# Kernel optimization log

Measured on AMD Instinct MI355X. Metric: run time of the kernel, lower is better.

Reference implementation:

```python
import jax, jax.numpy as jnp
from jax import lax
import numpy as np

# pywt Wavelet('db4') decomposition filters
DEC_LO = jnp.array([-0.010597401784997278, 0.032883011666982945, 0.030841381835986965,
                    -0.18703481171888114, -0.027983769416983848, 0.6308807679295904,
                    0.7148465705525415, 0.23037781330885523], dtype=jnp.float32)
DEC_HI = jnp.array([-0.23037781330885523, 0.7148465705525415, -0.6308807679295904,
                    -0.027983769416983848, 0.18703481171888114, 0.030841381835986965,
                    -0.032883011666982945, -0.010597401784997278], dtype=jnp.float32)
FLT = 8
BN_INV = np.float32(1.0 / np.sqrt(1.0 + 1e-5))  # BatchNorm eval: running_mean=0, running_var=1


def dwt_db4(v):
    """Vectorized pywt.dwt(v, 'db4', mode='symmetric') along the last axis.
    v: (..., n) -> (cA, cD), each (..., (n+FLT-1)//2).
    pywt: symmetric-pad by FLT-1, true convolution with filter, take valid[1::2].
    Equivalent: correlate padded[1:...] with flipped filter, stride 2."""
    n = v.shape[-1]
    out_len = (n + FLT - 1) // 2
    xp = jnp.pad(v, [(0, 0)] * (v.ndim - 1) + [(FLT - 1, FLT - 1)], mode='symmetric')
    xp = xp[..., 1:1 + 2 * (out_len - 1) + FLT]
    lead = v.shape[:-1]
    xr = xp.reshape(-1, 1, xp.shape[-1])                      # (N*, 1, L)
    kern = jnp.stack([DEC_LO[::-1], DEC_HI[::-1]])[:, None, :]  # (2, 1, 8)
    y = lax.conv_general_dilated(xr, kern, (2,), 'VALID',
                                 dimension_numbers=('NCH', 'OIH', 'NCH'))
    return y[:, 0].reshape(lead + (out_len,)), y[:, 1].reshape(lead + (out_len,))


def conv_bn_relu(x, w, g, b):
    # x: (B, C, S); w: (O, I, K) no bias; BN in eval mode; ReLU; dropout off (eval)
    k = w.shape[-1]
    p = (k - 1) // 2
    y = lax.conv_general_dilated(x, w, (1,), [(p, p)],
                                 dimension_numbers=('NCH', 'OIH', 'NCH'))
    return jax.nn.relu((g * BN_INV)[None, :, None] * y + b[None, :, None])


def setup_inputs() -> dict:
    key = jax.random.key(0)
    ks = jax.random.split(key, 16)
    C, S, B = 88, 2048, 4
    d = dict()
    d['x'] = jax.random.normal(ks[0], (B, S, C), dtype=jnp.float32)
    d['w1'] = jax.random.normal(ks[1], (C, C, 1), dtype=jnp.float32) * 0.05
    d['w2a'] = jax.random.normal(ks[2], (C, C, 1), dtype=jnp.float32) * 0.05
    d['w2b'] = jax.random.normal(ks[3], (C, C, 3), dtype=jnp.float32) * 0.05
    d['w3a'] = jax.random.normal(ks[4], (C, C, 1), dtype=jnp.float32) * 0.05
    d['w3b'] = jax.random.normal(ks[5], (C, C, 3), dtype=jnp.float32) * 0.05
    d['w3c'] = jax.random.normal(ks[6], (C, C, 5), dtype=jnp.float32) * 0.05
    for nm in ['g1', 'g2a', 'g2b', 'g3a', 'g3b', 'g3c']:
        d[nm] = jnp.ones((C,), dtype=jnp.float32)
    for nm in ['b1', 'b2a', 'b2b', 'b3a', 'b3b', 'b3c']:
        d[nm] = jnp.zeros((C,), dtype=jnp.float32)
    d['Wmp'] = jax.random.normal(ks[7], (C, 3 * C), dtype=jnp.float32) * 0.05
    d['bmp'] = jnp.zeros((C,), dtype=jnp.float32)
    d['Wq'] = jax.random.normal(ks[8], (C, C), dtype=jnp.float32) * 0.1
    d['Wk'] = jax.random.normal(ks[9], (C, C), dtype=jnp.float32) * 0.1
    d['Wv'] = jax.random.normal(ks[10], (C, C), dtype=jnp.float32) * 0.1
    d['Wout'] = jax.random.normal(ks[11], (C, 112), dtype=jnp.float32) * 0.05
    d['bout'] = jnp.zeros((C,), dtype=jnp.float32)
    return d


def reference(x, w1, g1, b1, w2a, g2a, b2a, w2b, g2b, b2b,
              w3a, g3a, b3a, w3b, g3b, b3b, w3c, g3c, b3c,
              Wmp, bmp, Wq, Wk, Wv, Wout, bout):
    B, S, H = x.shape
    head = 4
    dk = H // head                                # 22
    wd = dk // 2 + 3 if dk % 2 == 0 else (dk + 1) // 2 + 3  # 14
    xt = jnp.swapaxes(x, 1, 2)                    # (B, C, S)
    # mutil_Parallel: three conv lines + fuse + residual
    x1 = conv_bn_relu(xt, w1, g1, b1)
    x2 = conv_bn_relu(conv_bn_relu(xt, w2a, g2a, b2a), w2b, g2b, b2b)
    x3 = conv_bn_relu(conv_bn_relu(conv_bn_relu(xt, w3a, g3a, b3a), w3b, g3b, b3b), w3c, g3c, b3c)
    cat = jnp.concatenate([x1, x2, x3], axis=1)   # (B, 3C, S)
    mp = jnp.einsum('bcs,oc->bso', cat, Wmp) + bmp + x  # (B, S, C)
    identity = mp
    # multi-head attention with wavelet-transformed values
    scale = dk ** (-0.5)
    q = jnp.einsum('bsh,oh->bso', mp, Wq).reshape(B, S, head, dk).transpose(0, 2, 1, 3) * scale
    k = jnp.einsum('bsh,oh->bso', mp, Wk).reshape(B, S, head, dk).transpose(0, 2, 1, 3)
    v = jnp.einsum('bsh,oh->bso', mp, Wv).reshape(B, S, head, dk).transpose(0, 2, 1, 3)
    attn = jax.nn.softmax(jnp.einsum('bhqd,bhkd->bhqk', q, k), axis=-1)  # (B,4,S,S)
    cA, cD = dwt_db4(v)                           # each (B, 4, S, 14)
    wcd = jnp.einsum('bhqk,bhkd->bhqd', attn, cD)  # (B, 4, S, 14)
    xo = jax.nn.relu(wcd.transpose(0, 2, 1, 3).reshape(B, S, head * wd))
    cAr = cA.reshape(B, S, head * wd)             # faithful to source's direct .view
    out = jnp.concatenate([xo, cAr], axis=-1) @ Wout.T + bout
    return identity + out
```

## Files before the change

### kernel.cpp

```cpp
#include <hip/hip_runtime.h>

#define BN_INV  0.99999500003749981f
#define QSCALE  0.21320071635561041f

typedef unsigned int uint;
typedef unsigned short u16;
typedef __attribute__((ext_vector_type(8))) short s16x8;
typedef __attribute__((ext_vector_type(4))) float f32x4;

#define OFF_BCAT 0
#define OFF_V    512
#define OFF_MP   721408
#define SW0    2884608
#define SB1    (SW0)
#define SB2B   (SW0+30720)
#define SB3B   (SW0+67584)
#define SB3C   (SW0+104448)
#define SBMP   (SW0+165888)
#define SBQKV  (SW0+202752)
#define SBOUT  (SW0+239616)
#define SXB    3148800
#define SXCAT  3869696
#define SX2    6032384
#define ST3B   6753280
#define SX3    7474176
#define SMPB   8195072
#define SQB    3869696
#define SKB    4918272
#define SCDT   5966848
#define SXOB   6753280

__constant__ float c_dlo[8] = {-0.010597401784997278f, 0.032883011666982945f,
    0.030841381835986965f, -0.18703481171888114f, -0.02798376941698385f,
    0.6308807679295904f, 0.7148465705525415f, 0.23037781330885523f};
__constant__ float c_dhi[8] = {-0.23037781330885523f, 0.7148465705525415f,
    -0.6308807679295904f, -0.02798376941698385f, 0.18703481171888114f,
    0.030841381835986965f, -0.032883011666982945f, -0.010597401784997278f};

__device__ __forceinline__ u16 f2bf(float f) {
    uint u = __float_as_uint(f);
    uint r = u + 0x7fffu + ((u >> 16) & 1u);
    return (u16)(r >> 16);
}

__global__ __launch_bounds__(256) void prepk(
    const float* __restrict__ x,
    const float* __restrict__ w1, const float* __restrict__ w2a, const float* __restrict__ w2b,
    const float* __restrict__ w3a, const float* __restrict__ w3b, const float* __restrict__ w3c,
    const float* __restrict__ g1, const float* __restrict__ g2a, const float* __restrict__ g2b,
    const float* __restrict__ g3a, const float* __restrict__ g3b, const float* __restrict__ g3c,
    const float* __restrict__ b1, const float* __restrict__ b2a, const float* __restrict__ b3a,
    const float* __restrict__ Wmp, const float* __restrict__ Wq, const float* __restrict__ Wk,
    const float* __restrict__ Wv, const float* __restrict__ Wout, float* __restrict__ ws)
{
    u16* wu = (u16*)ws;
    int r = blockIdx.x * 256 + threadIdx.x;
    if (r < 264) {
        ws[OFF_BCAT + r] = (r < 88) ? b1[r] : (r < 176 ? b2a[r-88] : b3a[r-176]);
        return;
    }
    r -= 264;
    if (r < 320*96) {
        int n = r / 96, kk = r % 96; float v = 0.f;
        if (kk < 88 && n < 264) {
            if (n < 88)       v = w1 [n*88+kk]       * g1 [n];
            else if (n < 176) v = w2a[(n-88)*88+kk]  * g2a[n-88];
            else              v = w3a[(n-176)*88+kk] * g3a[n-176];
            v *= BN_INV;
        }
        wu[SB1 + r] = f2bf(v); return;
    }
    r -= 320*96;
    if (r < 128*288) {
        int n = r / 288, kk = r % 288, t = kk/96, i = kk%96; float v = 0.f;
        if (n < 88 && i < 88) v = w2b[n*264 + i*3 + t] * g2b[n] * BN_INV;
        wu[SB2B + r] = f2bf(v); return;
    }
    r -= 128*288;
    if (r < 128*288) {
        int n = r / 288, kk = r % 288, t = kk/96, i = kk%96; float v = 0.f;
        if (n < 88 && i < 88) v = w3b[n*264 + i*3 + t] * g3b[n] * BN_INV;
        wu[SB3B + r] = f2bf(v); return;
    }
    r -= 128*288;
    if (r < 128*480) {
        int n = r / 480, kk = r % 480, t = kk/96, i = kk%96; float v = 0.f;
        if (n < 88 && i < 88) v = w3c[n*440 + i*5 + t] * g3c[n] * BN_INV;
        wu[SB3C + r] = f2bf(v); return;
    }
    r -= 128*480;
    if (r < 128*288) {
        int n = r / 288, kk = r % 288, c = kk/96, i = kk%96; float v = 0.f;
        if (n < 88 && i < 88) v = Wmp[n*264 + c*88 + i];
        wu[SBMP + r] = f2bf(v); return;
    }
    r -= 128*288;
    if (r < 384*96) {
        int n = r / 96, kk = r % 96, sec = n / 128, o = n % 128; float v = 0.f;
        if (o < 88 && kk < 88) {
            if (sec == 0)      v = Wq[o*88+kk] * QSCALE;
            else if (sec == 1) v = Wk[o*88+kk];
            else               v = Wv[o*88+kk];
        }
        wu[SBQKV + r] = f2bf(v); return;
    }
    r -= 384*96;
    if (r < 128*192) {
        int n = r / 192, kk = r % 192; float v = 0.f;
        if (n < 88 && kk < 112) v = Wout[n*112 + kk];
        wu[SBOUT + r] = f2bf(v); return;
    }
    r -= 128*192;
    if (r < 8192*88) {
        wu[SXB + r] = f2bf(x[r]); return;
    }
}

struct GemmChunks {
    int soff[5];
    int stride[5];
    int shift[5];
    int cols[5];
};

template<int NCH, int MODE, int OUTM>
__global__ __launch_bounds__(256) void gemmk(GemmChunks ch,
    const u16* __restrict__ wsrc,
    const u16* __restrict__ Bw, const u16* __restrict__ Bw2, int Ktot,
    const float* __restrict__ bias, const float* __restrict__ bias2,
    const float* __restrict__ resid, int relu,
    u16* __restrict__ outb, u16* __restrict__ outb2,
    float* __restrict__ outf, int outStride, int N)
{
    __shared__ u16 As[64*104];
    __shared__ u16 Bs[64*104];
    int tid = threadIdx.x;
    int lane = tid & 63, w = tid >> 6, wr = w >> 1, wc = w & 1;
    int p0 = blockIdx.x * 64;
    int nb = blockIdx.y;
    int which = (MODE == 2) ? (nb >> 1) : 0;
    int nbl   = (MODE == 2) ? (nb & 1) : nb;
    const u16* Bw_ = (MODE == 2 && which) ? Bw2 : Bw;
    int bs = p0 & ~2047, be = bs + 2048;

    f32x4 acc[2][2];
    #pragma unroll
    for (int a = 0; a < 2; a++)
        #pragma unroll
        for (int b = 0; b < 2; b++) acc[a][b] = (f32x4){0.f,0.f,0.f,0.f};

    int ar0 = (wr*32 + (lane&15))*104 + (lane>>4)*8;
    int br0 = (wc*32 + (lane&15))*104 + (lane>>4)*8;

    int4 ra[3], rb[3];
    auto loadC = [&](int c) {
        int soff = ch.soff[c] + which*88;
        int stride = ch.stride[c], shift = ch.shift[c], cols = ch.cols[c];
        #pragma unroll
        for (int t = 0; t < 3; t++) {
            int e = tid + t*256;
            int r = e / 12, seg = e % 12;
            int row = p0 + r + shift;
            int4 v = {0,0,0,0};
            if (row >= bs && row < be && seg*8 < cols)
                v = *(const int4*)&wsrc[(size_t)soff + (size_t)row*stride + seg*8];
            ra[t] = v;
            rb[t] = *(const int4*)&Bw_[((size_t)(nbl*64 + r))*Ktot + c*96 + seg*8];
        }
    };

    loadC(0);
    for (int c = 0; c < NCH; c++) {
        #pragma unroll
        for (int t = 0; t < 3; t++) {
            int e = tid + t*256;
            int r = e / 12, seg = e % 12;
            *(int4*)&As[r*104 + seg*8] = ra[t];
            *(int4*)&Bs[r*104 + seg*8] = rb[t];
        }
        __syncthreads();
        if (c + 1 < NCH) loadC(c + 1);
        #pragma unroll
        for (int ks = 0; ks < 3; ks++) {
            s16x8 a0 = *(const s16x8*)&As[ar0 + ks*32];
            s16x8 a1 = *(const s16x8*)&As[ar0 + 16*104 + ks*32];
            s16x8 b0 = *(const s16x8*)&Bs[br0 + ks*32];
            s16x8 b1 = *(const s16x8*)&Bs[br0 + 16*104 + ks*32];
            acc[0][0] = __builtin_amdgcn_mfma_f32_16x16x32_bf16(a0, b0, acc[0][0], 0, 0, 0);
            acc[0][1] = __builtin_amdgcn_mfma_f32_16x16x32_bf16(a0, b1, acc[0][1], 0, 0, 0);
            acc[1][0] = __builtin_amdgcn_mfma_f32_16x16x32_bf16(a1, b0, acc[1][0], 0, 0, 0);
            acc[1][1] = __builtin_amdgcn_mfma_f32_16x16x32_bf16(a1, b1, acc[1][1], 0, 0, 0);
        }
        __syncthreads();
    }

    int rbase = p0 + wr*32 + (lane>>4)*4;
    if (MODE != 1) {
        u16* outb_ = (MODE == 2 && which) ? outb2 : outb;
        const float* bias_ = (MODE == 2 && which) ? bias2 : bias;
        int cbase = nbl*64 + wc*32 + (lane&15);
        #pragma unroll
        for (int fn = 0; fn < 2; fn++) {
            int col = cbase + fn*16;
            if (col < N) {
                float bb = bias_ ? bias_[col] : 0.f;
                #pragma unroll
                for (int fm = 0; fm < 2; fm++)
                    #pragma unroll
                    for (int j = 0; j < 4; j++) {
                        int row = rbase + fm*16 + j;
                        float v = acc[fm][fn][j] + bb;
                        if (relu) v = fmaxf(v, 0.f);
                        if (resid) v += resid[(size_t)row*outStride + col];
                        if (OUTM & 1) outb_[(size_t)row*outStride + col] = f2bf(v);
                        if (OUTM & 2) outf[(size_t)row*outStride + col] = v;
                    }
            }
        }
    } else {
        u16* wq = outb;
        int sec = nb >> 1;
        #pragma unroll
        for (int fn = 0; fn < 2; fn++) {
            int cw = (nb&1)*64 + wc*32 + fn*16 + (lane&15);
            if (cw < 88) {
                int h = cw / 22, d = cw % 22;
                #pragma unroll
                for (int fm = 0; fm < 2; fm++)
                    #pragma unroll
                    for (int j = 0; j < 4; j++) {
                        int row = rbase + fm*16 + j;
                        int b = row >> 11, s = row & 2047;
                        float v = acc[fm][fn][j];
                        if (sec == 0)
                            wq[SQB + ((size_t)(b*4+h)*2048 + s)*32 + d] = f2bf(v);
                        else if (sec == 1)
                            wq[SKB + ((size_t)(b*4+h)*2048 + s)*32 + d] = f2bf(v);
                        else
                            outf[OFF_V + (size_t)row*88 + cw] = v;
                    }
            }
        }
    }
}

__global__ __launch_bounds__(256) void dwtk(float* __restrict__ ws)
{
    u16* wu = (u16*)ws;
    int tid = threadIdx.x;
    int p0 = blockIdx.x * 16;
    const float* V = ws + OFF_V;
    for (int e = tid; e < 896; e += 256) {
        int p = e / 56, rr = e % 56, h = rr / 14, jj = rr % 14;
        int pos = p0 + p, b = pos >> 11, s = pos & 2047;
        const float* v = &V[(size_t)pos*88 + h*22];
        float ca = 0.f, cd = 0.f;
        #pragma unroll
        for (int t = 0; t < 8; t++) {
            int pp = 1 + 2*jj + t;
            int oi = pp < 7 ? 6 - pp : (pp < 29 ? pp - 7 : 50 - pp);
            float vv = v[oi];
            ca = fmaf(vv, c_dlo[7-t], ca);
            cd = fmaf(vv, c_dhi[7-t], cd);
        }
        wu[SCDT + ((size_t)((b*4+h)*16 + jj))*2048 + s] = f2bf(cd);
        int hs = h*2048 + s, s2 = hs >> 2, qd = hs & 3;
        wu[SXOB + ((size_t)b*2048 + s2)*112 + 56 + qd*14 + jj] = f2bf(ca);
    }
    uint* wi = (uint*)ws;
    for (int e = tid; e < 640; e += 256) {
        int p = e / 40, t = e % 40;
        int h = t / 10, rest = t % 10, arr = rest / 5, ui = rest % 5;
        int pos = p0 + p, b = pos >> 11, s = pos & 2047;
        size_t base = (size_t)((arr ? SKB : SQB) >> 1) + ((size_t)(b*4+h)*2048 + s)*16;
        wi[base + 11 + ui] = 0;
    }
    for (int e = tid; e < 128; e += 256) {
        int p = e / 8, t = e % 8, h = t >> 1, dd = 14 + (t & 1);
        int pos = p0 + p, b = pos >> 11, s = pos & 2047;
        wu[SCDT + ((size_t)((b*4+h)*16 + dd))*2048 + s] = 0;
    }
}

__global__ __launch_bounds__(512, 4) void attnk(float* __restrict__ ws)
{
    const u16* wu = (const u16*)ws;
    u16* wua = (u16*)ws;
    __shared__ __align__(16) u16 Kt[2*64*40];
    __shared__ __align__(16) u16 CDt[2*16*72];
    __shared__ __align__(16) u16 Pb[8][16*72];
    __shared__ float cb[8][16];
    int tid = threadIdx.x, lane = tid & 63, w = tid >> 6;
    int bh = blockIdx.y;
    int qsub = w & 3, half = w >> 2;
    int q0 = blockIdx.x * 64 + qsub * 16;
    int qrow = lane & 15, grp = lane >> 4;

    s16x8 qf = *(const s16x8*)&wu[SQB + ((size_t)bh*2048 + q0 + qrow)*32 + grp*8];
    const u16* Kbase = wu + SKB + (size_t)bh*2048*32;
    const u16* Cbase = wu + SCDT + (size_t)bh*16*2048;
    const u16* Kh = &Kt[half*2560];
    const u16* Ch = &CDt[half*1152];

    f32x4 o = (f32x4){0.f,0.f,0.f,0.f};
    float m = -1e30f, l = 0.f;

    for (int kt = 0; kt < 16; kt++) {
        __syncthreads();
        {
            int hh = tid >> 8, rr = (tid >> 2) & 63, seg = tid & 3;
            *(int4*)&Kt[hh*2560 + rr*40 + seg*8] =
                *(const int4*)&Kbase[(size_t)(hh*1024 + kt*64 + rr)*32 + seg*8];
        }
        if (tid < 256) {
            int hh = tid >> 7, d = (tid >> 3) & 15, seg = tid & 7;
            *(int4*)&CDt[hh*1152 + d*72 + seg*8] =
                *(const int4*)&Cbase[(size_t)d*2048 + hh*1024 + kt*64 + seg*8];
        }
        __syncthreads();

        f32x4 s4[4];
        #pragma unroll
        for (int sub = 0; sub < 4; sub++) {
            s16x8 kf = *(const s16x8*)&Kh[(sub*16 + qrow)*40 + grp*8];
            s4[sub] = __builtin_amdgcn_mfma_f32_16x16x32_bf16(kf, qf,
                        (f32x4){0.f,0.f,0.f,0.f}, 0, 0, 0);
        }
        float sv[16];
        #pragma unroll
        for (int sub = 0; sub < 4; sub++)
            #pragma unroll
            for (int j = 0; j < 4; j++) sv[sub*4+j] = s4[sub][j];

        float mx[8];
        #pragma unroll
        for (int i = 0; i < 8; i++) mx[i] = fmaxf(sv[i], sv[i+8]);
        #pragma unroll
        for (int i = 0; i < 4; i++) mx[i] = fmaxf(mx[i], mx[i+4]);
        float tm = fmaxf(fmaxf(mx[0], mx[1]), fmaxf(mx[2], mx[3]));
        tm = fmaxf(tm, __shfl_xor(tm, 16));
        tm = fmaxf(tm, __shfl_xor(tm, 32));

        if (!__all(tm <= m + 8.f)) {
            float mn = fmaxf(m, tm);
            float corr = __expf(m - mn);
            m = mn; l *= corr;
            if (lane < 16) cb[w][lane] = corr;
            __builtin_amdgcn_s_waitcnt(0);
            const float* cp = &cb[w][grp*4];
            #pragma unroll
            for (int j = 0; j < 4; j++) o[j] *= cp[j];
        }

        float pv[16];
        #pragma unroll
        for (int i = 0; i < 16; i++) pv[i] = __expf(sv[i] - m);
        float sm[8];
        #pragma unroll
        for (int i = 0; i < 8; i++) sm[i] = pv[i] + pv[i+8];
        #pragma unroll
        for (int i = 0; i < 4; i++) sm[i] += sm[i+4];
        float ls = (sm[0] + sm[1]) + (sm[2] + sm[3]);
        ls += __shfl_xor(ls, 16);
        ls += __shfl_xor(ls, 32);
        l += ls;

        {
            uint* pb32 = (uint*)Pb[w];
            #pragma unroll
            for (int sub = 0; sub < 4; sub++) {
                uint u01 = (uint)f2bf(pv[sub*4+0]) | ((uint)f2bf(pv[sub*4+1]) << 16);
                uint u23 = (uint)f2bf(pv[sub*4+2]) | ((uint)f2bf(pv[sub*4+3]) << 16);
                int sa = qrow*72 + sub*16 + grp*4;
                *(uint2*)&pb32[sa >> 1] = make_uint2(u01, u23);
            }
        }
        #pragma unroll
        for (int ks = 0; ks < 2; ks++) {
            s16x8 pa = *(const s16x8*)&Pb[w][qrow*72 + ks*32 + grp*8];
            s16x8 cf = *(const s16x8*)&Ch[qrow*72 + ks*32 + grp*8];
            o = __builtin_amdgcn_mfma_f32_16x16x32_bf16(pa, cf, o, 0, 0, 0);
        }
    }

    __syncthreads();
    float* part = (float*)Kt;
    if (lane < 16) { part[(w*16+lane)*18 + 0] = m; part[(w*16+lane)*18 + 1] = l; }
    #pragma unroll
    for (int j = 0; j < 4; j++) part[(w*16 + grp*4 + j)*18 + 2 + qrow] = o[j];
    __syncthreads();
    if (w < 4) {
        int q = qrow;
        const float* pa = &part[(w*16 + q)*18];
        const float* pb = &part[((w+4)*16 + q)*18];
        float m0 = pa[0], l0 = pa[1], m1 = pb[0], l1 = pb[1];
        float M = fmaxf(m0, m1);
        float e0 = __expf(m0 - M), e1 = __expf(m1 - M);
        float inv = 1.f / (l0*e0 + l1*e1);
        int b = bh >> 2, h = bh & 3;
        int s = blockIdx.x * 64 + w * 16 + q;
        #pragma unroll
        for (int dd = 0; dd < 4; dd++) {
            int d = grp*4 + dd;
            if (d < 14) {
                float val = (pa[2+d]*e0 + pb[2+d]*e1) * inv;
                wua[SXOB + ((size_t)b*2048 + s)*112 + h*14 + d] = f2bf(fmaxf(val, 0.f));
            }
        }
    }
}

extern "C" void kernel_launch(void* const* d_in, const int* in_sizes, int n_in,
                              void* d_out, int out_size, void* d_ws, size_t ws_size,
                              hipStream_t stream) {
    const float* x    = (const float*)d_in[0];
    const float* w1   = (const float*)d_in[1];
    const float* w2a  = (const float*)d_in[2];
    const float* w2b  = (const float*)d_in[3];
    const float* w3a  = (const float*)d_in[4];
    const float* w3b  = (const float*)d_in[5];
    const float* w3c  = (const float*)d_in[6];
    const float* g1   = (const float*)d_in[7];
    const float* g2a  = (const float*)d_in[8];
    const float* g2b  = (const float*)d_in[9];
    const float* g3a  = (const float*)d_in[10];
    const float* g3b  = (const float*)d_in[11];
    const float* g3c  = (const float*)d_in[12];
    const float* b1   = (const float*)d_in[13];
    const float* b2a  = (const float*)d_in[14];
    const float* b2b  = (const float*)d_in[15];
    const float* b3a  = (const float*)d_in[16];
    const float* b3b  = (const float*)d_in[17];
    const float* b3c  = (const float*)d_in[18];
    const float* Wmp  = (const float*)d_in[19];
    const float* bmp  = (const float*)d_in[20];
    const float* Wq   = (const float*)d_in[21];
    const float* Wk   = (const float*)d_in[22];
    const float* Wv   = (const float*)d_in[23];
    const float* Wout = (const float*)d_in[24];
    const float* bout = (const float*)d_in[25];
    float* ws = (float*)d_ws;
    float* out = (float*)d_out;
    u16* wu = (u16*)d_ws;

    prepk<<<3850, 256, 0, stream>>>(x, w1, w2a, w2b, w3a, w3b, w3c,
                                    g1, g2a, g2b, g3a, g3b, g3c,
                                    b1, b2a, b3a, Wmp, Wq, Wk, Wv, Wout, ws);

    {
        GemmChunks c{}; c.soff[0]=SXB; c.stride[0]=88; c.shift[0]=0; c.cols[0]=88;
        gemmk<1,0,1><<<dim3(128,5), 256, 0, stream>>>(c, wu, wu+SB1, nullptr, 96,
            ws+OFF_BCAT, nullptr, nullptr, 1, wu+SXCAT, nullptr, nullptr, 264, 264);
    }
    {
        GemmChunks c{};
        for (int t = 0; t < 3; t++) { c.soff[t]=SXCAT+88; c.stride[t]=264; c.shift[t]=t-1; c.cols[t]=88; }
        gemmk<3,2,1><<<dim3(128,4), 256, 0, stream>>>(c, wu, wu+SB2B, wu+SB3B, 288,
            b2b, b3b, nullptr, 1, wu+SX2, wu+ST3B, nullptr, 88, 88);
    }
    {
        GemmChunks c{};
        for (int t = 0; t < 5; t++) { c.soff[t]=ST3B; c.stride[t]=88; c.shift[t]=t-2; c.cols[t]=88; }
        gemmk<5,0,1><<<dim3(128,2), 256, 0, stream>>>(c, wu, wu+SB3C, nullptr, 480,
            b3c, nullptr, nullptr, 1, wu+SX3, nullptr, nullptr, 88, 88);
    }
    {
        GemmChunks c{};
        c.soff[0]=SXCAT; c.stride[0]=264; c.shift[0]=0; c.cols[0]=88;
        c.soff[1]=SX2;   c.stride[1]=88;  c.shift[1]=0; c.cols[1]=88;
        c.soff[2]=SX3;   c.stride[2]=88;  c.shift[2]=0; c.cols[2]=88;
        gemmk<3,0,3><<<dim3(128,2), 256, 0, stream>>>(c, wu, wu+SBMP, nullptr, 288,
            bmp, nullptr, x, 0, wu+SMPB, nullptr, ws+OFF_MP, 88, 88);
    }
    {
        GemmChunks c{}; c.soff[0]=SMPB; c.stride[0]=88; c.shift[0]=0; c.cols[0]=88;
        gemmk<1,1,0><<<dim3(128,6), 256, 0, stream>>>(c, wu, wu+SBQKV, nullptr, 96,
            nullptr, nullptr, nullptr, 0, wu, nullptr, ws, 0, 0);
    }
    dwtk<<<512, 256, 0, stream>>>(ws);
    attnk<<<dim3(32, 16), 512, 0, stream>>>(ws);
    {
        GemmChunks c{};
        c.soff[0]=SXOB;    c.stride[0]=112; c.shift[0]=0; c.cols[0]=96;
        c.soff[1]=SXOB+96; c.stride[1]=112; c.shift[1]=0; c.cols[1]=16;
        gemmk<2,0,2><<<dim3(128,2), 256, 0, stream>>>(c, wu, wu+SBOUT, nullptr, 192,
            bout, nullptr, ws+OFF_MP, 0, nullptr, nullptr, out, 88, 88);
    }
}
```

Baseline: 202.9 us.

## Split attention keys four ways, stage DWT input in LDS, move pad zeroing to GEMM

The attention kernel now gives each block 32 queries and splits the key range into four quarters across wave pairs. This doubles the grid to 1024 blocks and halves the serial key-tile loop, and the four partial softmax states are merged at the end. The DWT kernel stages 32 positions of V in shared memory with coalesced loads before computing the coefficients. Zeroing of the Q/K padding columns moves into the QKV GEMM epilogue, which removes scattered writes from the DWT kernel. In exchange, each block reloads its Q tile, uses more shared memory, and does a heavier four-way combine.

```diff
diff --git a/kernel.cpp b/kernel.cpp
--- a/kernel.cpp
+++ b/kernel.cpp
@@ -239,6 +239,17 @@
                         else
                             outf[OFF_V + (size_t)row*88 + cw] = v;
                     }
+            } else if (sec < 2 && cw < 128) {
+                int t = cw - 88, h = t / 10, dpad = 22 + t % 10;
+                size_t sqk = (sec == 0) ? (size_t)SQB : (size_t)SKB;
+                #pragma unroll
+                for (int fm = 0; fm < 2; fm++)
+                    #pragma unroll
+                    for (int j = 0; j < 4; j++) {
+                        int row = rbase + fm*16 + j;
+                        int b = row >> 11, s = row & 2047;
+                        wq[sqk + ((size_t)(b*4+h)*2048 + s)*32 + dpad] = 0;
+                    }
             }
         }
     }
@@ -247,13 +258,22 @@
 __global__ __launch_bounds__(256) void dwtk(float* __restrict__ ws)
 {
     u16* wu = (u16*)ws;
+    __shared__ float vs[32*89];
     int tid = threadIdx.x;
-    int p0 = blockIdx.x * 16;
+    int p0 = blockIdx.x * 32;
     const float* V = ws + OFF_V;
-    for (int e = tid; e < 896; e += 256) {
-        int p = e / 56, rr = e % 56, h = rr / 14, jj = rr % 14;
-        int pos = p0 + p, b = pos >> 11, s = pos & 2047;
-        const float* v = &V[(size_t)pos*88 + h*22];
+    for (int e = tid; e < 32*88; e += 256) {
+        int p = e / 88, c = e - p*88;
+        vs[p*89 + c] = V[(size_t)p0*88 + e];
+    }
+    __syncthreads();
+    int b = p0 >> 11, sbase = p0 & 2047;
+    #pragma unroll
+    for (int it = 0; it < 7; it++) {
+        int idx = it*256 + tid;
+        int p = idx & 31, hjj = idx >> 5;
+        int h = hjj / 14, jj = hjj - h*14;
+        const float* v = &vs[p*89 + h*22];
         float ca = 0.f, cd = 0.f;
         #pragma unroll
         for (int t = 0; t < 8; t++) {
@@ -263,22 +283,15 @@
             ca = fmaf(vv, c_dlo[7-t], ca);
             cd = fmaf(vv, c_dhi[7-t], cd);
         }
+        int s = sbase + p;
         wu[SCDT + ((size_t)((b*4+h)*16 + jj))*2048 + s] = f2bf(cd);
         int hs = h*2048 + s, s2 = hs >> 2, qd = hs & 3;
         wu[SXOB + ((size_t)b*2048 + s2)*112 + 56 + qd*14 + jj] = f2bf(ca);
     }
-    uint* wi = (uint*)ws;
-    for (int e = tid; e < 640; e += 256) {
-        int p = e / 40, t = e % 40;
-        int h = t / 10, rest = t % 10, arr = rest / 5, ui = rest % 5;
-        int pos = p0 + p, b = pos >> 11, s = pos & 2047;
-        size_t base = (size_t)((arr ? SKB : SQB) >> 1) + ((size_t)(b*4+h)*2048 + s)*16;
-        wi[base + 11 + ui] = 0;
-    }
-    for (int e = tid; e < 128; e += 256) {
-        int p = e / 8, t = e % 8, h = t >> 1, dd = 14 + (t & 1);
-        int pos = p0 + p, b = pos >> 11, s = pos & 2047;
-        wu[SCDT + ((size_t)((b*4+h)*16 + dd))*2048 + s] = 0;
+    {
+        int p = tid & 31, t = tid >> 5;
+        int h = t >> 1, dd = 14 + (t & 1);
+        wu[SCDT + ((size_t)((b*4+h)*16 + dd))*2048 + sbase + p] = 0;
     }
 }
 
@@ -286,36 +299,38 @@
 {
     const u16* wu = (const u16*)ws;
     u16* wua = (u16*)ws;
-    __shared__ __align__(16) u16 Kt[2*64*40];
-    __shared__ __align__(16) u16 CDt[2*16*72];
+    __shared__ __align__(16) u16 Kt[4*64*40];
+    __shared__ __align__(16) u16 CDt[4*16*72];
     __shared__ __align__(16) u16 Pb[8][16*72];
     __shared__ float cb[8][16];
     int tid = threadIdx.x, lane = tid & 63, w = tid >> 6;
     int bh = blockIdx.y;
-    int qsub = w & 3, half = w >> 2;
-    int q0 = blockIdx.x * 64 + qsub * 16;
+    int qsub = w & 1, quar = w >> 1;
+    int q0 = blockIdx.x * 32 + qsub * 16;
     int qrow = lane & 15, grp = lane >> 4;
 
     s16x8 qf = *(const s16x8*)&wu[SQB + ((size_t)bh*2048 + q0 + qrow)*32 + grp*8];
     const u16* Kbase = wu + SKB + (size_t)bh*2048*32;
     const u16* Cbase = wu + SCDT + (size_t)bh*16*2048;
-    const u16* Kh = &Kt[half*2560];
-    const u16* Ch = &CDt[half*1152];
+    const u16* Kh = &Kt[quar*2560];
+    const u16* Ch = &CDt[quar*1152];
 
     f32x4 o = (f32x4){0.f,0.f,0.f,0.f};
     float m = -1e30f, l = 0.f;
 
-    for (int kt = 0; kt < 16; kt++) {
+    for (int kt = 0; kt < 8; kt++) {
         __syncthreads();
+        #pragma unroll
+        for (int t = 0; t < 2; t++) {
+            int e = tid + t*512;
+            int qq = e >> 8, rr = (e >> 2) & 63, seg = e & 3;
+            *(int4*)&Kt[qq*2560 + rr*40 + seg*8] =
+                *(const int4*)&Kbase[(size_t)(qq*512 + kt*64 + rr)*32 + seg*8];
+        }
         {
-            int hh = tid >> 8, rr = (tid >> 2) & 63, seg = tid & 3;
-            *(int4*)&Kt[hh*2560 + rr*40 + seg*8] =
-                *(const int4*)&Kbase[(size_t)(hh*1024 + kt*64 + rr)*32 + seg*8];
-        }
-        if (tid < 256) {
-            int hh = tid >> 7, d = (tid >> 3) & 15, seg = tid & 7;
-            *(int4*)&CDt[hh*1152 + d*72 + seg*8] =
-                *(const int4*)&Cbase[(size_t)d*2048 + hh*1024 + kt*64 + seg*8];
+            int qq = tid >> 7, d = (tid >> 3) & 15, seg = tid & 7;
+            *(int4*)&CDt[qq*1152 + d*72 + seg*8] =
+                *(const int4*)&Cbase[(size_t)d*2048 + qq*512 + kt*64 + seg*8];
         }
         __syncthreads();
 
@@ -389,23 +404,28 @@
     #pragma unroll
     for (int j = 0; j < 4; j++) part[(w*16 + grp*4 + j)*18 + 2 + qrow] = o[j];
     __syncthreads();
-    if (w < 4) {
+    if (w < 2) {
         int q = qrow;
-        const float* pa = &part[(w*16 + q)*18];
-        const float* pb = &part[((w+4)*16 + q)*18];
-        float m0 = pa[0], l0 = pa[1], m1 = pb[0], l1 = pb[1];
-        float M = fmaxf(m0, m1);
-        float e0 = __expf(m0 - M), e1 = __expf(m1 - M);
-        float inv = 1.f / (l0*e0 + l1*e1);
+        float M = -1e30f;
+        #pragma unroll
+        for (int qt = 0; qt < 4; qt++) M = fmaxf(M, part[((qt*2+w)*16 + q)*18]);
+        float L = 0.f, v[4] = {0.f,0.f,0.f,0.f};
+        #pragma unroll
+        for (int qt = 0; qt < 4; qt++) {
+            const float* pp = &part[((qt*2+w)*16 + q)*18];
+            float ee = __expf(pp[0] - M);
+            L += ee * pp[1];
+            #pragma unroll
+            for (int dd = 0; dd < 4; dd++) v[dd] += ee * pp[2 + grp*4 + dd];
+        }
+        float inv = 1.f / L;
         int b = bh >> 2, h = bh & 3;
-        int s = blockIdx.x * 64 + w * 16 + q;
+        int s = blockIdx.x * 32 + w * 16 + q;
         #pragma unroll
         for (int dd = 0; dd < 4; dd++) {
             int d = grp*4 + dd;
-            if (d < 14) {
-                float val = (pa[2+d]*e0 + pb[2+d]*e1) * inv;
-                wua[SXOB + ((size_t)b*2048 + s)*112 + h*14 + d] = f2bf(fmaxf(val, 0.f));
-            }
+            if (d < 14)
+                wua[SXOB + ((size_t)b*2048 + s)*112 + h*14 + d] = f2bf(fmaxf(v[dd]*inv, 0.f));
         }
     }
 }
@@ -477,8 +497,8 @@
         gemmk<1,1,0><<<dim3(128,6), 256, 0, stream>>>(c, wu, wu+SBQKV, nullptr, 96,
             nullptr, nullptr, nullptr, 0, wu, nullptr, ws, 0, 0);
     }
-    dwtk<<<512, 256, 0, stream>>>(ws);
-    attnk<<<dim3(32, 16), 512, 0, stream>>>(ws);
+    dwtk<<<256, 256, 0, stream>>>(ws);
+    attnk<<<dim3(64, 16), 512, 0, stream>>>(ws);
     {
         GemmChunks c{};
         c.soff[0]=SXOB;    c.stride[0]=112; c.shift[0]=0; c.cols[0]=96;
```

Measured after the change: 204.9 us. About the same (+1.0%).

## Stage GEMM conv halos in LDS once, prefetch attention tiles, stage DWT input

Applied to the files above, without the earlier changes.

The conv-as-GEMM kernel now loads the whole input tile plus a halo of neighbouring rows, and all weight chunks, into shared memory in one pass. Each shifted tap then reuses those rows instead of reloading shifted copies per chunk, and the per-chunk barriers go away. The attention kernel register-prefetches the next K and CD tiles and broadcasts the softmax correction with a shuffle instead of through shared memory. The DWT kernel stages V rows in shared memory, processes 32 positions per block, and moves zeroing of the Q/K padding columns into the QKV GEMM epilogue. The costs are more shared memory per GEMM block, which may lower occupancy, and the loss of load/compute overlap inside the GEMM.

```diff
diff --git a/kernel.cpp b/kernel.cpp
--- a/kernel.cpp
+++ b/kernel.cpp
@@ -119,21 +119,23 @@
 struct GemmChunks {
     int soff[5];
     int stride[5];
-    int shift[5];
     int cols[5];
 };
 
-template<int NCH, int MODE, int OUTM>
+template<int NCH, int HALO, int MODE, int OUTM>
 __global__ __launch_bounds__(256) void gemmk(GemmChunks ch,
     const u16* __restrict__ wsrc,
-    const u16* __restrict__ Bw, const u16* __restrict__ Bw2, int Ktot,
+    const u16* __restrict__ Bw, const u16* __restrict__ Bw2,
     const float* __restrict__ bias, const float* __restrict__ bias2,
     const float* __restrict__ resid, int relu,
     u16* __restrict__ outb, u16* __restrict__ outb2,
     float* __restrict__ outf, int outStride, int N)
 {
-    __shared__ u16 As[64*104];
-    __shared__ u16 Bs[64*104];
+    constexpr int RA   = HALO ? (64 + NCH - 1) : 64 * NCH;
+    constexpr int BSTR = NCH * 96 + 8;
+    constexpr int KTOT = NCH * 96;
+    __shared__ u16 As[RA * 104];
+    __shared__ u16 Bs[64 * BSTR];
     int tid = threadIdx.x;
     int lane = tid & 63, w = tid >> 6, wr = w >> 1, wc = w & 1;
     int p0 = blockIdx.x * 64;
@@ -143,6 +145,36 @@
     const u16* Bw_ = (MODE == 2 && which) ? Bw2 : Bw;
     int bs = p0 & ~2047, be = bs + 2048;
 
+    if (HALO) {
+        constexpr int OFS = (NCH - 1) / 2;
+        int soff = ch.soff[0] + which * 88;
+        int stride = ch.stride[0], cols = ch.cols[0];
+        for (int e = tid; e < RA * 12; e += 256) {
+            int r = e / 12, seg = e % 12;
+            int row = p0 + r - OFS;
+            int4 v = {0,0,0,0};
+            if (row >= bs && row < be && seg*8 < cols)
+                v = *(const int4*)&wsrc[(size_t)soff + (size_t)row*stride + seg*8];
+            *(int4*)&As[r*104 + seg*8] = v;
+        }
+    } else {
+        for (int e = tid; e < NCH * 768; e += 256) {
+            int c = e / 768, rem = e - c*768;
+            int r = rem / 12, seg = rem % 12;
+            int row = p0 + r;
+            int4 v = {0,0,0,0};
+            if (seg*8 < ch.cols[c])
+                v = *(const int4*)&wsrc[(size_t)ch.soff[c] + (size_t)row*ch.stride[c] + seg*8];
+            *(int4*)&As[c*6656 + r*104 + seg*8] = v;
+        }
+    }
+    for (int e = tid; e < 64 * NCH * 12; e += 256) {
+        int n = e / (NCH*12), seg = e % (NCH*12);
+        *(int4*)&Bs[n*BSTR + seg*8] =
+            *(const int4*)&Bw_[((size_t)(nbl*64 + n))*KTOT + seg*8];
+    }
+    __syncthreads();
+
     f32x4 acc[2][2];
     #pragma unroll
     for (int a = 0; a < 2; a++)
@@ -150,48 +182,23 @@
         for (int b = 0; b < 2; b++) acc[a][b] = (f32x4){0.f,0.f,0.f,0.f};
 
     int ar0 = (wr*32 + (lane&15))*104 + (lane>>4)*8;
-    int br0 = (wc*32 + (lane&15))*104 + (lane>>4)*8;
-
-    int4 ra[3], rb[3];
-    auto loadC = [&](int c) {
-        int soff = ch.soff[c] + which*88;
-        int stride = ch.stride[c], shift = ch.shift[c], cols = ch.cols[c];
-        #pragma unroll
-        for (int t = 0; t < 3; t++) {
-            int e = tid + t*256;
-            int r = e / 12, seg = e % 12;
-            int row = p0 + r + shift;
-            int4 v = {0,0,0,0};
-            if (row >= bs && row < be && seg*8 < cols)
-                v = *(const int4*)&wsrc[(size_t)soff + (size_t)row*stride + seg*8];
-            ra[t] = v;
-            rb[t] = *(const int4*)&Bw_[((size_t)(nbl*64 + r))*Ktot + c*96 + seg*8];
-        }
-    };
-
-    loadC(0);
+    int br0 = (wc*32 + (lane&15))*BSTR + (lane>>4)*8;
+
+    #pragma unroll
     for (int c = 0; c < NCH; c++) {
-        #pragma unroll
-        for (int t = 0; t < 3; t++) {
-            int e = tid + t*256;
-            int r = e / 12, seg = e % 12;
-            *(int4*)&As[r*104 + seg*8] = ra[t];
-            *(int4*)&Bs[r*104 + seg*8] = rb[t];
-        }
-        __syncthreads();
-        if (c + 1 < NCH) loadC(c + 1);
+        int abase = HALO ? (ar0 + c*104) : (c*6656 + ar0);
+        int bbase = br0 + c*96;
         #pragma unroll
         for (int ks = 0; ks < 3; ks++) {
-            s16x8 a0 = *(const s16x8*)&As[ar0 + ks*32];
-            s16x8 a1 = *(const s16x8*)&As[ar0 + 16*104 + ks*32];
-            s16x8 b0 = *(const s16x8*)&Bs[br0 + ks*32];
-            s16x8 b1 = *(const s16x8*)&Bs[br0 + 16*104 + ks*32];
+            s16x8 a0 = *(const s16x8*)&As[abase + ks*32];
+            s16x8 a1 = *(const s16x8*)&As[abase + 16*104 + ks*32];
+            s16x8 b0 = *(const s16x8*)&Bs[bbase + ks*32];
+            s16x8 b1 = *(const s16x8*)&Bs[bbase + 16*BSTR + ks*32];
             acc[0][0] = __builtin_amdgcn_mfma_f32_16x16x32_bf16(a0, b0, acc[0][0], 0, 0, 0);
             acc[0][1] = __builtin_amdgcn_mfma_f32_16x16x32_bf16(a0, b1, acc[0][1], 0, 0, 0);
             acc[1][0] = __builtin_amdgcn_mfma_f32_16x16x32_bf16(a1, b0, acc[1][0], 0, 0, 0);
             acc[1][1] = __builtin_amdgcn_mfma_f32_16x16x32_bf16(a1, b1, acc[1][1], 0, 0, 0);
         }
-        __syncthreads();
     }
 
     int rbase = p0 + wr*32 + (lane>>4)*4;
@@ -239,6 +246,17 @@
                         else
                             outf[OFF_V + (size_t)row*88 + cw] = v;
                     }
+            } else if (sec < 2 && cw < 128) {
+                int t = cw - 88, h = t / 10, dpad = 22 + t % 10;
+                size_t sqk = (sec == 0) ? (size_t)SQB : (size_t)SKB;
+                #pragma unroll
+                for (int fm = 0; fm < 2; fm++)
+                    #pragma unroll
+                    for (int j = 0; j < 4; j++) {
+                        int row = rbase + fm*16 + j;
+                        int b = row >> 11, s = row & 2047;
+                        wq[sqk + ((size_t)(b*4+h)*2048 + s)*32 + dpad] = 0;
+                    }
             }
         }
     }
@@ -247,13 +265,22 @@
 __global__ __launch_bounds__(256) void dwtk(float* __restrict__ ws)
 {
     u16* wu = (u16*)ws;
+    __shared__ float vs[32*89];
     int tid = threadIdx.x;
-    int p0 = blockIdx.x * 16;
+    int p0 = blockIdx.x * 32;
     const float* V = ws + OFF_V;
-    for (int e = tid; e < 896; e += 256) {
-        int p = e / 56, rr = e % 56, h = rr / 14, jj = rr % 14;
-        int pos = p0 + p, b = pos >> 11, s = pos & 2047;
-        const float* v = &V[(size_t)pos*88 + h*22];
+    for (int e = tid; e < 32*88; e += 256) {
+        int p = e / 88, c = e - p*88;
+        vs[p*89 + c] = V[(size_t)p0*88 + e];
+    }
+    __syncthreads();
+    int b = p0 >> 11, sbase = p0 & 2047;
+    #pragma unroll
+    for (int it = 0; it < 7; it++) {
+        int idx = it*256 + tid;
+        int p = idx & 31, hjj = idx >> 5;
+        int h = hjj / 14, jj = hjj - h*14;
+        const float* v = &vs[p*89 + h*22];
         float ca = 0.f, cd = 0.f;
         #pragma unroll
         for (int t = 0; t < 8; t++) {
@@ -263,22 +290,15 @@
             ca = fmaf(vv, c_dlo[7-t], ca);
             cd = fmaf(vv, c_dhi[7-t], cd);
         }
+        int s = sbase + p;
         wu[SCDT + ((size_t)((b*4+h)*16 + jj))*2048 + s] = f2bf(cd);
         int hs = h*2048 + s, s2 = hs >> 2, qd = hs & 3;
         wu[SXOB + ((size_t)b*2048 + s2)*112 + 56 + qd*14 + jj] = f2bf(ca);
     }
-    uint* wi = (uint*)ws;
-    for (int e = tid; e < 640; e += 256) {
-        int p = e / 40, t = e % 40;
-        int h = t / 10, rest = t % 10, arr = rest / 5, ui = rest % 5;
-        int pos = p0 + p, b = pos >> 11, s = pos & 2047;
-        size_t base = (size_t)((arr ? SKB : SQB) >> 1) + ((size_t)(b*4+h)*2048 + s)*16;
-        wi[base + 11 + ui] = 0;
-    }
-    for (int e = tid; e < 128; e += 256) {
-        int p = e / 8, t = e % 8, h = t >> 1, dd = 14 + (t & 1);
-        int pos = p0 + p, b = pos >> 11, s = pos & 2047;
-        wu[SCDT + ((size_t)((b*4+h)*16 + dd))*2048 + s] = 0;
+    {
+        int p = tid & 31, t = tid >> 5;
+        int h = t >> 1, dd = 14 + (t & 1);
+        wu[SCDT + ((size_t)((b*4+h)*16 + dd))*2048 + sbase + p] = 0;
     }
 }
 
@@ -289,7 +309,6 @@
     __shared__ __align__(16) u16 Kt[2*64*40];
     __shared__ __align__(16) u16 CDt[2*16*72];
     __shared__ __align__(16) u16 Pb[8][16*72];
-    __shared__ float cb[8][16];
     int tid = threadIdx.x, lane = tid & 63, w = tid >> 6;
     int bh = blockIdx.y;
     int qsub = w & 3, half = w >> 2;
@@ -302,22 +321,27 @@
     const u16* Kh = &Kt[half*2560];
     const u16* Ch = &CDt[half*1152];
 
+    int khh = tid >> 8, krr = (tid >> 2) & 63, kseg = tid & 3;
+    int chh = tid >> 7, cdd = (tid >> 3) & 15, cseg = tid & 7;
+
     f32x4 o = (f32x4){0.f,0.f,0.f,0.f};
     float m = -1e30f, l = 0.f;
 
+    int4 kreg = *(const int4*)&Kbase[(size_t)(khh*1024 + krr)*32 + kseg*8];
+    int4 creg = {0,0,0,0};
+    if (tid < 256)
+        creg = *(const int4*)&Cbase[(size_t)cdd*2048 + chh*1024 + cseg*8];
+
     for (int kt = 0; kt < 16; kt++) {
         __syncthreads();
-        {
-            int hh = tid >> 8, rr = (tid >> 2) & 63, seg = tid & 3;
-            *(int4*)&Kt[hh*2560 + rr*40 + seg*8] =
-                *(const int4*)&Kbase[(size_t)(hh*1024 + kt*64 + rr)*32 + seg*8];
-        }
-        if (tid < 256) {
-            int hh = tid >> 7, d = (tid >> 3) & 15, seg = tid & 7;
-            *(int4*)&CDt[hh*1152 + d*72 + seg*8] =
-                *(const int4*)&Cbase[(size_t)d*2048 + hh*1024 + kt*64 + seg*8];
-        }
+        *(int4*)&Kt[khh*2560 + krr*40 + kseg*8] = kreg;
+        if (tid < 256) *(int4*)&CDt[chh*1152 + cdd*72 + cseg*8] = creg;
         __syncthreads();
+        if (kt < 15) {
+            kreg = *(const int4*)&Kbase[(size_t)(khh*1024 + (kt+1)*64 + krr)*32 + kseg*8];
+            if (tid < 256)
+                creg = *(const int4*)&Cbase[(size_t)cdd*2048 + chh*1024 + (kt+1)*64 + cseg*8];
+        }
 
         f32x4 s4[4];
         #pragma unroll
@@ -345,11 +369,8 @@
             float mn = fmaxf(m, tm);
             float corr = __expf(m - mn);
             m = mn; l *= corr;
-            if (lane < 16) cb[w][lane] = corr;
-            __builtin_amdgcn_s_waitcnt(0);
-            const float* cp = &cb[w][grp*4];
             #pragma unroll
-            for (int j = 0; j < 4; j++) o[j] *= cp[j];
+            for (int j = 0; j < 4; j++) o[j] *= __shfl(corr, grp*4 + j);
         }
 
         float pv[16];
@@ -448,42 +469,40 @@
                                     b1, b2a, b3a, Wmp, Wq, Wk, Wv, Wout, ws);
 
     {
-        GemmChunks c{}; c.soff[0]=SXB; c.stride[0]=88; c.shift[0]=0; c.cols[0]=88;
-        gemmk<1,0,1><<<dim3(128,5), 256, 0, stream>>>(c, wu, wu+SB1, nullptr, 96,
+        GemmChunks c{}; c.soff[0]=SXB; c.stride[0]=88; c.cols[0]=88;
+        gemmk<1,1,0,1><<<dim3(128,5), 256, 0, stream>>>(c, wu, wu+SB1, nullptr,
             ws+OFF_BCAT, nullptr, nullptr, 1, wu+SXCAT, nullptr, nullptr, 264, 264);
     }
     {
+        GemmChunks c{}; c.soff[0]=SXCAT+88; c.stride[0]=264; c.cols[0]=88;
+        gemmk<3,1,2,1><<<dim3(128,4), 256, 0, stream>>>(c, wu, wu+SB2B, wu+SB3B,
+            b2b, b3b, nullptr, 1, wu+SX2, wu+ST3B, nullptr, 88, 88);
+    }
+    {
+        GemmChunks c{}; c.soff[0]=ST3B; c.stride[0]=88; c.cols[0]=88;
+        gemmk<5,1,0,1><<<dim3(128,2), 256, 0, stream>>>(c, wu, wu+SB3C, nullptr,
+            b3c, nullptr, nullptr, 1, wu+SX3, nullptr, nullptr, 88, 88);
+    }
+    {
         GemmChunks c{};
-        for (int t = 0; t < 3; t++) { c.soff[t]=SXCAT+88; c.stride[t]=264; c.shift[t]=t-1; c.cols[t]=88; }
-        gemmk<3,2,1><<<dim3(128,4), 256, 0, stream>>>(c, wu, wu+SB2B, wu+SB3B, 288,
-            b2b, b3b, nullptr, 1, wu+SX2, wu+ST3B, nullptr, 88, 88);
-    }
+        c.soff[0]=SXCAT; c.stride[0]=264; c.cols[0]=88;
+        c.soff[1]=SX2;   c.stride[1]=88;  c.cols[1]=88;
+        c.soff[2]=SX3;   c.stride[2]=88;  c.cols[2]=88;
+        gemmk<3,0,0,3><<<dim3(128,2), 256, 0, stream>>>(c, wu, wu+SBMP, nullptr,
+            bmp, nullptr, x, 0, wu+SMPB, nullptr, ws+OFF_MP, 88, 88);
+    }
+    {
+        GemmChunks c{}; c.soff[0]=SMPB; c.stride[0]=88; c.cols[0]=88;
+        gemmk<1,1,1,0><<<dim3(128,6), 256, 0, stream>>>(c, wu, wu+SBQKV, nullptr,
+            nullptr, nullptr, nullptr, 0, wu, nullptr, ws, 0, 0);
+    }
+    dwtk<<<256, 256, 0, stream>>>(ws);
+    attnk<<<dim3(32, 16), 512, 0, stream>>>(ws);
     {
         GemmChunks c{};
-        for (int t = 0; t < 5; t++) { c.soff[t]=ST3B; c.stride[t]=88; c.shift[t]=t-2; c.cols[t]=88; }
-        gemmk<5,0,1><<<dim3(128,2), 256, 0, stream>>>(c, wu, wu+SB3C, nullptr, 480,
-            b3c, nullptr, nullptr, 1, wu+SX3, nullptr, nullptr, 88, 88);
-    }
-    {
-        GemmChunks c{};
-        c.soff[0]=SXCAT; c.stride[0]=264; c.shift[0]=0; c.cols[0]=88;
-        c.soff[1]=SX2;   c.stride[1]=88;  c.shift[1]=0; c.cols[1]=88;
-        c.soff[2]=SX3;   c.stride[2]=88;  c.shift[2]=0; c.cols[2]=88;
-        gemmk<3,0,3><<<dim3(128,2), 256, 0, stream>>>(c, wu, wu+SBMP, nullptr, 288,
-            bmp, nullptr, x, 0, wu+SMPB, nullptr, ws+OFF_MP, 88, 88);
-    }
-    {
-        GemmChunks c{}; c.soff[0]=SMPB; c.stride[0]=88; c.shift[0]=0; c.cols[0]=88;
-        gemmk<1,1,0><<<dim3(128,6), 256, 0, stream>>>(c, wu, wu+SBQKV, nullptr, 96,
-            nullptr, nullptr, nullptr, 0, wu, nullptr, ws, 0, 0);
-    }
-    dwtk<<<512, 256, 0, stream>>>(ws);
-    attnk<<<dim3(32, 16), 512, 0, stream>>>(ws);
-    {
-        GemmChunks c{};
-        c.soff[0]=SXOB;    c.stride[0]=112; c.shift[0]=0; c.cols[0]=96;
-        c.soff[1]=SXOB+96; c.stride[1]=112; c.shift[1]=0; c.cols[1]=16;
-        gemmk<2,0,2><<<dim3(128,2), 256, 0, stream>>>(c, wu, wu+SBOUT, nullptr, 192,
+        c.soff[0]=SXOB;    c.stride[0]=112; c.cols[0]=96;
+        c.soff[1]=SXOB+96; c.stride[1]=112; c.cols[1]=16;
+        gemmk<2,0,0,2><<<dim3(128,2), 256, 0, stream>>>(c, wu, wu+SBOUT, nullptr,
             bout, nullptr, ws+OFF_MP, 0, nullptr, nullptr, out, 88, 88);
     }
 }
```

Result: faster. 197.3 us (-2.8%).
